# Optimization experiments

Hardware: AMD Instinct MI355X
Metric: run time of the kernel (lower is better)

The kernel has to match this reference:

```python
import jax, jax.numpy as jnp
import numpy as np

EPS = 1e-5

def layer_norm(x, g, b):
    m = jnp.mean(x, axis=-1, keepdims=True)
    v = jnp.mean((x - m) ** 2, axis=-1, keepdims=True)
    return (x - m) * jax.lax.rsqrt(v + EPS) * g + b

def conv1d(x, w, b, pad):
    # x: [B, C_in, L], w: [C_out, C_in, K]
    y = jax.lax.conv_general_dilated(x, w, (1,), [(pad, pad)],
                                     dimension_numbers=('NCH', 'OIH', 'NCH'))
    return y + b[None, :, None]

def setup_inputs() -> dict:
    key = jax.random.key(0)
    B, L, D, H, W, HID = 8, 1024, 512, 8, 3, 64
    ks = jax.random.split(key, 32)
    s = 0.02
    inp = {}
    inp['x'] = jax.random.normal(ks[0], (B, L, D), jnp.float32)
    # WaveDetector convs
    inp['conv1_w'] = jax.random.normal(ks[1], (HID, D, 5), jnp.float32) * s
    inp['conv1_b'] = jnp.zeros((HID,), jnp.float32)
    inp['conv2_w'] = jax.random.normal(ks[2], (HID, HID, 3), jnp.float32) * s
    inp['conv2_b'] = jnp.zeros((HID,), jnp.float32)
    inp['conv3_w'] = jax.random.normal(ks[3], (W, HID, 3), jnp.float32) * s
    inp['conv3_b'] = jnp.zeros((W,), jnp.float32)
    # wave type embedding
    inp['wave_emb'] = jax.random.normal(ks[4], (W, D), jnp.float32) * s
    # attention projections (stored as [in, out])
    inp['wq_w'] = jax.random.normal(ks[5], (D, D), jnp.float32) * s
    inp['wq_b'] = jnp.zeros((D,), jnp.float32)
    inp['wk_w'] = jax.random.normal(ks[6], (D, D), jnp.float32) * s
    inp['wk_b'] = jnp.zeros((D,), jnp.float32)
    inp['wv_w'] = jax.random.normal(ks[7], (D, D), jnp.float32) * s
    inp['wv_b'] = jnp.zeros((D,), jnp.float32)
    # gate MLP: D -> D//4 -> H
    inp['g1_w'] = jax.random.normal(ks[8], (D, D // 4), jnp.float32) * s
    inp['g1_b'] = jnp.zeros((D // 4,), jnp.float32)
    inp['g2_w'] = jax.random.normal(ks[9], (D // 4, H), jnp.float32) * s
    inp['g2_b'] = jnp.zeros((H,), jnp.float32)
    # layer norms
    for i, nm in enumerate(['ln_attn', 'norm1', 'ln_conv', 'norm2', 'norm3']):
        inp[nm + '_g'] = jnp.ones((D,), jnp.float32) + jax.random.normal(ks[10 + i], (D,), jnp.float32) * 0.01
        inp[nm + '_b'] = jax.random.normal(ks[15 + i], (D,), jnp.float32) * 0.01
    # subgraph conv: one Linear per wave + wave weights
    inp['wc_w'] = jax.random.normal(ks[20], (W, D, D), jnp.float32) * s
    inp['wc_b'] = jnp.zeros((W, D), jnp.float32)
    inp['wave_weights'] = jnp.ones((W,), jnp.float32) / W
    # FFN
    inp['f1_w'] = jax.random.normal(ks[21], (D, 4 * D), jnp.float32) * s
    inp['f1_b'] = jnp.zeros((4 * D,), jnp.float32)
    inp['f2_w'] = jax.random.normal(ks[22], (4 * D, D), jnp.float32) * s
    inp['f2_b'] = jnp.zeros((D,), jnp.float32)
    return inp

def reference(x, conv1_w, conv1_b, conv2_w, conv2_b, conv3_w, conv3_b, wave_emb,
              wq_w, wq_b, wk_w, wk_b, wv_w, wv_b, g1_w, g1_b, g2_w, g2_b,
              ln_attn_g, ln_attn_b, norm1_g, norm1_b, wc_w, wc_b, wave_weights,
              ln_conv_g, ln_conv_b, norm2_g, norm2_b, f1_w, f1_b, f2_w, f2_b,
              norm3_g, norm3_b):
    B, L, D = x.shape
    H = g2_w.shape[1]
    hd = D // H
    # --- WaveDetector ---
    xt = jnp.swapaxes(x, 1, 2)                       # [B, D, L]
    h = jax.nn.relu(conv1d(xt, conv1_w, conv1_b, 2))
    h = jax.nn.relu(conv1d(h, conv2_w, conv2_b, 1))
    wp = conv1d(h, conv3_w, conv3_b, 1)              # [B, W, L]
    wave_mask = jax.nn.softmax(jnp.swapaxes(wp, 1, 2), axis=-1)  # [B, L, W]
    # --- WaveTypeEncoding ---
    labels = jnp.argmax(wave_mask, axis=-1)          # [B, L] int
    x = x + wave_emb[labels]
    # --- subgraph adjacency (base_adj = ones) ---
    wave_sim = jnp.einsum('blw,bmw->blm', wave_mask, wave_mask)  # [B, L, L]
    subgraph_adj = wave_sim
    # --- DynamicWaveAttention ---
    residual = x
    Q = (x @ wq_w + wq_b).reshape(B, L, H, hd)
    K = (x @ wk_w + wk_b).reshape(B, L, H, hd)
    V = (x @ wv_w + wv_b).reshape(B, L, H, hd)
    scores = jnp.einsum('bqhd,bkhd->bhqk', Q, K) / (hd ** 0.5)
    gates = jax.nn.sigmoid(jax.nn.relu(x @ g1_w + g1_b) @ g2_w + g2_b)  # [B, L, H]
    gates = jnp.transpose(gates, (0, 2, 1))[:, :, None, :]              # [B, H, 1, L]
    scores = scores * gates + scores * wave_sim[:, None]
    scores = scores + subgraph_adj[:, None]
    attn = jax.nn.softmax(scores, axis=-1)
    attn_out = jnp.einsum('bhqk,bkhd->bqhd', attn, V).reshape(B, L, D)
    attn_out = layer_norm(attn_out + residual, ln_attn_g, ln_attn_b)
    x = layer_norm(x + attn_out, norm1_g, norm1_b)
    # --- ECGSubGraphConv (adj_matrices=None path) ---
    feats = jnp.einsum('bld,wdo->blwo', x, wc_w) + wc_b          # [B, L, W, D]
    conv_out = jnp.einsum('blwo,blw,w->blo', feats, wave_mask, wave_weights)
    conv_out = layer_norm(jax.nn.relu(conv_out), ln_conv_g, ln_conv_b)
    x = layer_norm(x + conv_out, norm2_g, norm2_b)
    # --- FFN ---
    ffn = jax.nn.relu(x @ f1_w + f1_b) @ f2_w + f2_b
    x = layer_norm(x + ffn, norm3_g, norm3_b)
    return (x, wave_mask, subgraph_adj)
```

## Files before the change

### kernel.cpp

```cpp
#include <hip/hip_runtime.h>

typedef unsigned short u16;
typedef unsigned int u32;
typedef __attribute__((ext_vector_type(8))) short bf16x8;
typedef __attribute__((ext_vector_type(4))) float f32x4;
typedef __attribute__((ext_vector_type(4))) u32 u32x4;

#define DEVI static __device__ __forceinline__

constexpr size_t OFF_WTQKV = 0;
constexpr size_t OFF_G1T   = 1572864;
constexpr size_t OFF_G2T   = OFF_G1T + 131072;
constexpr size_t OFF_WCT   = OFF_G2T + 2048;
constexpr size_t OFF_F1T   = OFF_WCT + 1572864;
constexpr size_t OFF_F2T   = OFF_F1T + 2097152;
constexpr size_t OFF_W1R   = OFF_F2T + 2097152;
constexpr size_t OFF_W2R   = OFF_W1R + 655360;
constexpr size_t OFF_H1    = OFF_W2R + 49152;
constexpr size_t OFF_GMID  = OFF_H1;
constexpr size_t OFF_GATES = OFF_H1 + 2097152;
constexpr size_t OFF_X1    = OFF_GATES + 262144;
constexpr size_t OFF_X3    = OFF_X1;
constexpr size_t OFF_X1B   = OFF_X1 + 16777216;
constexpr size_t OFF_FMID  = OFF_X1B;
constexpr size_t OFF_Q     = OFF_X1B + 8388608;
constexpr size_t OFF_H1P   = OFF_Q;
constexpr size_t OFF_K     = OFF_Q + 8388608;
constexpr size_t OFF_XH    = OFF_K;
constexpr size_t OFF_VT    = OFF_K + 8388608;
constexpr size_t OFF_XL    = OFF_VT + 32768;
constexpr size_t OFF_AO    = OFF_VT + 8388608;
constexpr size_t OFF_CONV  = OFF_AO;
constexpr size_t OFF_FP0   = OFF_AO;
constexpr size_t OFF_X2    = OFF_AO + 16777216;
constexpr size_t OFF_FP1   = OFF_X2;
constexpr size_t OFF_X2B   = OFF_X2 + 16777216;
constexpr size_t OFF_X3B   = OFF_X2B;

DEVI u16 f2bf(float f) {
  u32 u = __builtin_bit_cast(u32, f);
  u32 r = (u + 0x7FFFu + ((u >> 16) & 1u)) >> 16;
  return (u16)r;
}
DEVI float bf2f(u16 h) { u32 u = ((u32)h) << 16; return __builtin_bit_cast(float, u); }

DEVI void load8(const float* __restrict__ p, float o[8]) {
  const float4* q = (const float4*)p;
  float4 a = q[0], b = q[1];
  o[0]=a.x; o[1]=a.y; o[2]=a.z; o[3]=a.w; o[4]=b.x; o[5]=b.y; o[6]=b.z; o[7]=b.w;
}
DEVI void store8(float* __restrict__ p, const float o[8]) {
  float4 a; a.x=o[0]; a.y=o[1]; a.z=o[2]; a.w=o[3];
  float4 b; b.x=o[4]; b.y=o[5]; b.z=o[6]; b.w=o[7];
  float4* q = (float4*)p; q[0]=a; q[1]=b;
}
DEVI void store8bf(u16* __restrict__ p, const float o[8]) {
  u32 w[4];
#pragma unroll
  for (int i=0;i<4;i++) w[i] = (u32)f2bf(o[2*i]) | ((u32)f2bf(o[2*i+1]) << 16);
  u32x4 v; v.x=w[0]; v.y=w[1]; v.z=w[2]; v.w=w[3];
  *(u32x4*)p = v;
}

DEVI void gl_lds16(const u16* g, u16* l) {
  __builtin_amdgcn_global_load_lds((const __attribute__((address_space(1))) u32*)g,
                                   (__attribute__((address_space(3))) u32*)l, 16, 0, 0);
}

#define PIPE_WAIT(N)  asm volatile("s_waitcnt vmcnt(%0)" :: "n"(N) : "memory")
#define PIPE_WAIT0()  asm volatile("s_waitcnt vmcnt(0)" ::: "memory")
#define PIPE_BAR()    do { __builtin_amdgcn_s_barrier(); asm volatile("" ::: "memory"); } while (0)
#define PIPE_BAR_LGKM() do { asm volatile("s_waitcnt lgkmcnt(0)" ::: "memory"); \
                             __builtin_amdgcn_s_barrier(); asm volatile("" ::: "memory"); } while (0)

__global__ __launch_bounds__(64) void prep_kernel(
    const float* s0, const float* s1, const float* s2, const float* s3, const float* s4,
    const float* s5, const float* s6, const float* s7, const float* s8, const float* s9,
    char* ws) {
  const int jsrc[11] = {0,1,2,3,4, 5,5,5, 6,7, 9};
  const int jK[11]   = {512,512,512,512,128, 512,512,512, 512,2048, 64};
  const int jN[11]   = {512,512,512,128,8,   512,512,512, 2048,512, 192};
  const int jSo[11]  = {0,0,0,0,0, 0,262144,524288, 0,0, 0};
  const long long jDo[11] = {
    (long long)OFF_WTQKV, (long long)(OFF_WTQKV+524288), (long long)(OFF_WTQKV+1048576),
    (long long)OFF_G1T, (long long)OFF_G2T,
    (long long)OFF_WCT, (long long)(OFF_WCT+524288), (long long)(OFF_WCT+1048576),
    (long long)OFF_F1T, (long long)OFF_F2T, (long long)OFF_W2R};
  const int jF[11]   = {0,0,0,0,0,0,0,0,0,0,1};

  int blk = blockIdx.x;
  int j = 0, t = 0;
  for (int i = 0; i < 11; i++) {
    int cnt = ((jK[i] + 63) >> 6) * ((jN[i] + 63) >> 6);
    if (blk < cnt) { j = i; t = blk; break; }
    blk -= cnt;
  }
  int K = jK[j], N = jN[j];
  int ktiles = (K + 63) >> 6;
  int k0 = (t % ktiles) << 6, n0 = (t / ktiles) << 6;
  const float* SS[10] = {s0,s1,s2,s3,s4,s5,s6,s7,s8,s9};
  const float* src = SS[jsrc[j]] + jSo[j];
  __shared__ float tile[64][65];
  int tt = threadIdx.x;
  for (int i = 0; i < 64; i++) {
    float v = 0.f;
    if (k0 + i < K && n0 + tt < N) v = src[(size_t)(k0 + i) * N + n0 + tt];
    tile[i][tt] = v;
  }
  __syncthreads();
  if (jF[j]) {
    float* dst = (float*)(ws + jDo[j]);
    for (int i = 0; i < 64; i++)
      if (n0 + i < N && k0 + tt < K) dst[(size_t)(n0 + i) * K + k0 + tt] = tile[tt][i];
  } else {
    u16* dst = (u16*)(ws + jDo[j]);
    for (int i = 0; i < 64; i++)
      if (n0 + i < N && k0 + tt < K) dst[(size_t)(n0 + i) * K + k0 + tt] = f2bf(tile[tt][i]);
  }
}

__global__ __launch_bounds__(256) void wprep_kernel(const float* __restrict__ w1,
                                                    u16* __restrict__ wh, u16* __restrict__ wl) {
  int c = blockIdx.x;
  for (int kk = threadIdx.x; kk < 2560; kk += 256) {
    int k = kk >> 9, d = kk & 511;
    float v = w1[(size_t)c * 2560 + d * 5 + k];
    u16 h = f2bf(v);
    wh[(size_t)c * 2560 + kk] = h;
    wl[(size_t)c * 2560 + kk] = f2bf(v - bf2f(h));
  }
}

__global__ __launch_bounds__(256) void xsplit_kernel(const float* __restrict__ x,
                                                     u16* __restrict__ xh, u16* __restrict__ xl) {
  int idx = blockIdx.x * 256 + threadIdx.x;
  if (idx >= 8 * 1028 * 64) return;
  int r = idx >> 6;
  int col = (idx & 63) * 8;
  int b = r / 1028, rr = r % 1028;
  size_t dof = ((size_t)r) * 512 + col;
  if (rr < 2 || rr >= 1026) {
    u32x4 z; z.x = 0; z.y = 0; z.z = 0; z.w = 0;
    *(u32x4*)&xh[dof] = z;
    *(u32x4*)&xl[dof] = z;
    return;
  }
  const float* src = x + (((size_t)b << 10) + rr - 2) * 512 + col;
  float v[8];
  load8(src, v);
  u32 wh_[4], wl_[4];
#pragma unroll
  for (int i = 0; i < 4; i++) {
    u16 h0 = f2bf(v[2 * i]),     l0 = f2bf(v[2 * i]     - bf2f(f2bf(v[2 * i])));
    u16 h1 = f2bf(v[2 * i + 1]), l1 = f2bf(v[2 * i + 1] - bf2f(f2bf(v[2 * i + 1])));
    wh_[i] = (u32)h0 | ((u32)h1 << 16);
    wl_[i] = (u32)l0 | ((u32)l1 << 16);
  }
  u32x4 H; H.x=wh_[0]; H.y=wh_[1]; H.z=wh_[2]; H.w=wh_[3];
  u32x4 L; L.x=wl_[0]; L.y=wl_[1]; L.z=wl_[2]; L.w=wl_[3];
  *(u32x4*)&xh[dof] = H;
  *(u32x4*)&xl[dof] = L;
}

__global__ __launch_bounds__(256, 6) void conv1g_kernel(
    const u16* __restrict__ xh, const u16* __restrict__ xl,
    const u16* __restrict__ wh, const u16* __restrict__ wl,
    float* __restrict__ h1p) {
  __shared__ alignas(16) u16 a_s[2][64 * 32];
  __shared__ alignas(16) u16 b_s[2][64 * 32];
  const int tid = threadIdx.x, lane = tid & 63, wid = tid >> 6;
  const int m0 = blockIdx.x * 64;
  const int z = blockIdx.z;
  const int wr = wid >> 1, wc = wid & 1;
  const int mb = wr * 32, nb = wc * 32;
  const int lrow = lane & 15, lk = (lane >> 4) * 8;
  const int lr4 = lane >> 2, lc8 = (lane & 3) * 8;
  const int bb = m0 >> 10, lblk = m0 & 1023;
  const size_t xrow0 = (size_t)bb * 1028;

  auto stage = [&](int buf, int kk) {
    int p = (kk >= 5120) ? 2 : (kk >= 2560) ? 1 : 0;
    int kpp = kk - p * 2560;
    int ktap = kpp >> 9, d0 = kpp & 511;
    const u16* xa = (p == 1) ? xl : xh;
    const u16* wb = (p == 2) ? wl : wh;
    gl_lds16(&xa[(xrow0 + lblk + wid * 16 + lr4 + ktap) * 512 + d0 + lc8],
             &a_s[buf][wid * 512]);
    gl_lds16(&wb[(size_t)(wid * 16 + lr4) * 2560 + kpp + lc8],
             &b_s[buf][wid * 512]);
  };

  f32x4 acc[2][2];
#pragma unroll
  for (int m = 0; m < 2; m++)
#pragma unroll
    for (int n = 0; n < 2; n++) { acc[m][n].x=0.f; acc[m][n].y=0.f; acc[m][n].z=0.f; acc[m][n].w=0.f; }

  const int kz0 = z * 1920, kz1 = kz0 + 1920;
  stage(0, kz0);
  int cur = 0;
  for (int kk = kz0; kk < kz1; kk += 32) {
    if (kk + 32 < kz1) {
      stage(cur ^ 1, kk + 32);
      PIPE_WAIT(2);
    } else {
      PIPE_WAIT0();
    }
    PIPE_BAR();
    bf16x8 af[2], bfr[2];
#pragma unroll
    for (int m = 0; m < 2; m++) af[m]  = *(const bf16x8*)&a_s[cur][(mb + m * 16 + lrow) * 32 + lk];
#pragma unroll
    for (int n = 0; n < 2; n++) bfr[n] = *(const bf16x8*)&b_s[cur][(nb + n * 16 + lrow) * 32 + lk];
#pragma unroll
    for (int m = 0; m < 2; m++)
#pragma unroll
      for (int n = 0; n < 2; n++)
        acc[m][n] = __builtin_amdgcn_mfma_f32_16x16x32_bf16(af[m], bfr[n], acc[m][n], 0, 0, 0);
    PIPE_BAR_LGKM();
    cur ^= 1;
  }
  const int r4 = (lane >> 4) * 4;
#pragma unroll
  for (int m = 0; m < 2; m++) {
#pragma unroll
    for (int n = 0; n < 2; n++) {
      const int col = nb + n * 16 + lrow;
#pragma unroll
      for (int j = 0; j < 4; j++) {
        const int row = m0 + mb + m * 16 + r4 + j;
        h1p[(size_t)z * 524288 + (size_t)row * 64 + col] = acc[m][n][j];
      }
    }
  }
}

__global__ __launch_bounds__(256) void conv23_kernel(
    const float* __restrict__ h1p, const float* __restrict__ b1,
    const float* __restrict__ w2r, const float* __restrict__ b2,
    const float* __restrict__ w3, const float* __restrict__ b3,
    const float* __restrict__ x, const float* __restrict__ emb,
    float* __restrict__ wmOut, float* __restrict__ x1, u16* __restrict__ x1b) {
  int seg = blockIdx.x;
  int batch = seg >> 6, l0 = (seg & 63) << 4;
  int tid = threadIdx.x, lane = tid & 63, wave = tid >> 6;
  __shared__ float hs[20][64];
  __shared__ float h2s[18][65];
  __shared__ float w3s[576];
  __shared__ int labS[16];
  for (int i = tid; i < 20 * 64; i += 256) {
    int r = i >> 6, cc = i & 63;
    int lp = l0 - 2 + r;
    float v = 0.f;
    if (lp >= 0 && lp < 1024) {
      size_t base = ((size_t)batch * 1024 + lp) * 64 + cc;
      float s = b1[cc];
#pragma unroll
      for (int q = 0; q < 4; q++) s += h1p[base + (size_t)q * 524288];
      v = fmaxf(s, 0.f);
    }
    hs[r][cc] = v;
  }
  for (int i = tid; i < 576; i += 256) w3s[i] = w3[i];
  __syncthreads();
  {
    int c = lane;
    int r0 = wave * 5;
    float a2[5];
#pragma unroll
    for (int i = 0; i < 5; i++) a2[i] = b2[c];
    for (int dd = 0; dd < 64; dd++) {
      float xv[7];
#pragma unroll
      for (int i = 0; i < 7; i++) xv[i] = (r0 + i < 20) ? hs[r0 + i][dd] : 0.f;
#pragma unroll
      for (int k = 0; k < 3; k++) {
        float wv = w2r[(size_t)(dd * 3 + k) * 64 + c];
#pragma unroll
        for (int i = 0; i < 5; i++) a2[i] += xv[i + k] * wv;
      }
    }
#pragma unroll
    for (int i = 0; i < 5; i++) {
      int hr = r0 + i;
      if (hr < 18) h2s[hr][c] = fmaxf(a2[i], 0.f);
    }
  }
  __syncthreads();
  {
    int li = tid >> 4, g = tid & 15;
    int c0 = g * 4;
    float wp[3];
#pragma unroll
    for (int jw = 0; jw < 3; jw++) {
      float a = 0.f;
#pragma unroll
      for (int k = 0; k < 3; k++)
#pragma unroll
        for (int c = 0; c < 4; c++)
          a += h2s[li + k][c0 + c] * w3s[(jw * 64 + c0 + c) * 3 + k];
      wp[jw] = a;
    }
#pragma unroll
    for (int d = 1; d < 16; d <<= 1) {
#pragma unroll
      for (int jw = 0; jw < 3; jw++) wp[jw] += __shfl_xor(wp[jw], d);
    }
    if (g == 0) {
      float wp0 = wp[0] + b3[0], wp1 = wp[1] + b3[1], wp2 = wp[2] + b3[2];
      float mx = fmaxf(wp0, fmaxf(wp1, wp2));
      float e0 = __expf(wp0 - mx), e1 = __expf(wp1 - mx), e2 = __expf(wp2 - mx);
      float inv = 1.f / (e0 + e1 + e2);
      size_t mo = ((size_t)batch * 1024 + l0 + li) * 3;
      wmOut[mo] = e0 * inv; wmOut[mo + 1] = e1 * inv; wmOut[mo + 2] = e2 * inv;
      int lb = 0; float bv = wp0;
      if (wp1 > bv) { bv = wp1; lb = 1; }
      if (wp2 > bv) { lb = 2; }
      labS[li] = lb;
    }
  }
  __syncthreads();
  for (int i = tid; i < 16 * 128; i += 256) {
    int r = i >> 7, cq = (i & 127) << 2;
    size_t gi = ((size_t)batch * 1024 + l0 + r) * 512 + cq;
    float4 xv = *(const float4*)&x[gi];
    const float* ep = &emb[(size_t)labS[r] * 512 + cq];
    float4 ev = *(const float4*)ep;
    float4 v; v.x = xv.x + ev.x; v.y = xv.y + ev.y; v.z = xv.z + ev.z; v.w = xv.w + ev.w;
    *(float4*)&x1[gi] = v;
    u32 lo = (u32)f2bf(v.x) | ((u32)f2bf(v.y) << 16);
    u32 hi = (u32)f2bf(v.z) | ((u32)f2bf(v.w) << 16);
    *(u32*)&x1b[gi] = lo;
    *(u32*)&x1b[gi + 2] = hi;
  }
}

__global__ __launch_bounds__(256) void wavesim_kernel(const float* __restrict__ wm,
                                                      float* __restrict__ adj) {
  int b = blockIdx.x >> 7;
  int r0 = (blockIdx.x & 127) << 3;
  __shared__ float ms[1024][3];
  int tid = threadIdx.x;
  for (int i = tid; i < 3072; i += 256) ms[i / 3][i % 3] = wm[(size_t)b * 3072 + i];
  __syncthreads();
  for (int r = 0; r < 8; r++) {
    float a0 = ms[r0 + r][0], a1 = ms[r0 + r][1], a2 = ms[r0 + r][2];
    for (int m = tid; m < 1024; m += 256)
      adj[((size_t)b * 1024 + r0 + r) * 1024 + m] = a0 * ms[m][0] + a1 * ms[m][1] + a2 * ms[m][2];
  }
}

struct GemmArgs {
  const u16* A; const u16* Bt;
  int lda; int ldb; int K;
  const float* bias;
  u16* obf; int ldo;
  float* of32; int ldo32;
  u16* Qo; u16* Ko; u16* Vto;
  const float* bq; const float* bk; const float* bv;
};

template<int BM, int BN, int FM, int FN, int EPI>
__global__ __launch_bounds__(256, 3) void gemm_k(GemmArgs p) {
  __shared__ alignas(16) u16 a_s[2][BM * 32];
  __shared__ alignas(16) u16 b_s[2][BN * 32];
  const int tid = threadIdx.x;
  const int lane = tid & 63, wid = tid >> 6;
  const int m0 = blockIdx.x * BM, n0 = blockIdx.y * BN;
  const int koff = (EPI == 6) ? blockIdx.z * p.K : 0;
  const int wr = wid >> 1, wc = wid & 1;
  const int mb = wr * (FM * 16), nb = wc * (FN * 16);
  const int lrow = lane & 15, lk = (lane >> 4) * 8;
  constexpr int CPW_A = BM / 64;
  constexpr int CPW_B = BN / 64;
  constexpr int NL = CPW_A + CPW_B;
  const int lr4 = lane >> 2, lc8 = (lane & 3) * 8;

  auto stage = [&](int buf, int k0) {
#pragma unroll
    for (int j = 0; j < CPW_A; j++) {
      int chunk = wid * CPW_A + j;
      gl_lds16(&p.A[(size_t)(m0 + chunk * 16 + lr4) * p.lda + koff + k0 + lc8],
               &a_s[buf][chunk * 512]);
    }
#pragma unroll
    for (int j = 0; j < CPW_B; j++) {
      int chunk = wid * CPW_B + j;
      gl_lds16(&p.Bt[(size_t)(n0 + chunk * 16 + lr4) * p.ldb + koff + k0 + lc8],
               &b_s[buf][chunk * 512]);
    }
  };

  f32x4 acc[FM][FN];
#pragma unroll
  for (int m = 0; m < FM; m++)
#pragma unroll
    for (int n = 0; n < FN; n++) { acc[m][n].x=0.f; acc[m][n].y=0.f; acc[m][n].z=0.f; acc[m][n].w=0.f; }

  stage(0, 0);
  int cur = 0;
  for (int k0 = 0; k0 < p.K; k0 += 32) {
    if (k0 + 32 < p.K) {
      stage(cur ^ 1, k0 + 32);
      PIPE_WAIT(NL);
    } else {
      PIPE_WAIT0();
    }
    PIPE_BAR();
    bf16x8 af[FM], bfr[FN];
#pragma unroll
    for (int m = 0; m < FM; m++) af[m] = *(const bf16x8*)&a_s[cur][(mb + m * 16 + lrow) * 32 + lk];
#pragma unroll
    for (int n = 0; n < FN; n++) bfr[n] = *(const bf16x8*)&b_s[cur][(nb + n * 16 + lrow) * 32 + lk];
#pragma unroll
    for (int m = 0; m < FM; m++)
#pragma unroll
      for (int n = 0; n < FN; n++)
        acc[m][n] = __builtin_amdgcn_mfma_f32_16x16x32_bf16(af[m], bfr[n], acc[m][n], 0, 0, 0);
    PIPE_BAR_LGKM();
    cur ^= 1;
  }
  const int r4 = (lane >> 4) * 4;
#pragma unroll
  for (int m = 0; m < FM; m++) {
#pragma unroll
    for (int n = 0; n < FN; n++) {
      const int col = n0 + nb + n * 16 + lrow;
#pragma unroll
      for (int j = 0; j < 4; j++) {
        const int row = m0 + mb + m * 16 + r4 + j;
        float v = acc[m][n][j];
        if constexpr (EPI == 1) {
          v += p.bias[col];
          v = fmaxf(v, 0.f);
          p.obf[(size_t)row * p.ldo + col] = f2bf(v);
        } else if constexpr (EPI == 2) {
          v += p.bias[col];
          p.of32[(size_t)row * p.ldo32 + col] = v;
        } else if constexpr (EPI == 3) {
          if (col < 512) {
            v += p.bq[col];
            p.Qo[(size_t)row * 512 + col] = f2bf(v);
          } else if (col < 1024) {
            int cc = col - 512;
            v += p.bk[cc];
            p.Ko[(size_t)row * 512 + cc] = f2bf(v);
          } else if (col < 1536) {
            int cc = col - 1024;
            v += p.bv[cc];
            int hh = cc >> 6, dd = cc & 63;
            int bb2 = row >> 10, ll = row & 1023;
            p.Vto[((((size_t)bb2 * 8 + hh) * 64 + dd) << 10) + ll] = f2bf(v);
          } else {
            int cc = col - 1536;
            v += p.bias[cc];
            v = fmaxf(v, 0.f);
            p.obf[(size_t)row * 128 + cc] = f2bf(v);
          }
        } else if constexpr (EPI == 6) {
          if (blockIdx.z == 0) v += p.bias[col];
          p.of32[(size_t)blockIdx.z * p.ldo32 + (size_t)row * 512 + col] = v;
        }
      }
    }
  }
}

__global__ __launch_bounds__(256) void wcg_kernel(
    const u16* __restrict__ A, const u16* __restrict__ Wct,
    const float* __restrict__ wcb, const float* __restrict__ wmask,
    const float* __restrict__ wwts, float* __restrict__ out) {
  __shared__ alignas(16) u16 a_s[2][128 * 32];
  __shared__ alignas(16) u16 b_s[2][3 * 64 * 32];
  const int tid = threadIdx.x, lane = tid & 63, wid = tid >> 6;
  const int m0 = blockIdx.x * 128, n0 = blockIdx.y * 64;
  const int wr = wid >> 1, wc = wid & 1;
  const int mb = wr * 64, nb = wc * 32;
  const int lrow = lane & 15, lk = (lane >> 4) * 8;
  const int lr4 = lane >> 2, lc8 = (lane & 3) * 8;

  auto stage = [&](int buf, int k0) {
#pragma unroll
    for (int t = 0; t < 2; t++) {
      int ch = wid * 2 + t;
      gl_lds16(&A[(size_t)(m0 + ch * 16 + lr4) * 512 + k0 + lc8], &a_s[buf][ch * 512]);
    }
#pragma unroll
    for (int t = 0; t < 3; t++) {
      int ch = wid * 3 + t;
      int wI = ch >> 2, sub = ch & 3;
      gl_lds16(&Wct[(size_t)wI * 262144 + (size_t)(n0 + sub * 16 + lr4) * 512 + k0 + lc8],
               &b_s[buf][ch * 512]);
    }
  };

  f32x4 acc[4][2][3];
#pragma unroll
  for (int m = 0; m < 4; m++)
#pragma unroll
    for (int n = 0; n < 2; n++)
#pragma unroll
      for (int w = 0; w < 3; w++) { acc[m][n][w].x=0.f; acc[m][n][w].y=0.f; acc[m][n][w].z=0.f; acc[m][n][w].w=0.f; }

  stage(0, 0);
  int cur = 0;
  for (int k0 = 0; k0 < 512; k0 += 32) {
    if (k0 + 32 < 512) {
      stage(cur ^ 1, k0 + 32);
      PIPE_WAIT(5);
    } else {
      PIPE_WAIT0();
    }
    PIPE_BAR();
    bf16x8 af[4], bfr[3][2];
#pragma unroll
    for (int m = 0; m < 4; m++) af[m] = *(const bf16x8*)&a_s[cur][(mb + m * 16 + lrow) * 32 + lk];
#pragma unroll
    for (int w = 0; w < 3; w++)
#pragma unroll
      for (int n = 0; n < 2; n++)
        bfr[w][n] = *(const bf16x8*)&b_s[cur][(w * 64 + nb + n * 16 + lrow) * 32 + lk];
#pragma unroll
    for (int m = 0; m < 4; m++)
#pragma unroll
      for (int n = 0; n < 2; n++)
#pragma unroll
        for (int w = 0; w < 3; w++)
          acc[m][n][w] = __builtin_amdgcn_mfma_f32_16x16x32_bf16(af[m], bfr[w][n], acc[m][n][w], 0, 0, 0);
    PIPE_BAR_LGKM();
    cur ^= 1;
  }
  const float w0 = wwts[0], w1 = wwts[1], w2 = wwts[2];
  const int r4 = (lane >> 4) * 4;
#pragma unroll
  for (int m = 0; m < 4; m++) {
#pragma unroll
    for (int j = 0; j < 4; j++) {
      const int row = m0 + mb + m * 16 + r4 + j;
      float c0 = wmask[(size_t)row * 3 + 0] * w0;
      float c1 = wmask[(size_t)row * 3 + 1] * w1;
      float c2 = wmask[(size_t)row * 3 + 2] * w2;
#pragma unroll
      for (int n = 0; n < 2; n++) {
        const int col = n0 + nb + n * 16 + lrow;
        float v = c0 * (acc[m][n][0][j] + wcb[col])
                + c1 * (acc[m][n][1][j] + wcb[512 + col])
                + c2 * (acc[m][n][2][j] + wcb[1024 + col]);
        out[(size_t)row * 512 + col] = v;
      }
    }
  }
}

__global__ __launch_bounds__(256) void gates2_kernel(const u16* __restrict__ gmid,
    const u16* __restrict__ g2t, const float* __restrict__ g2b, float* __restrict__ gates) {
  int r0 = blockIdx.x * 64;
  __shared__ u16 ms[64][136];
  __shared__ u16 gs[8][136];
  __shared__ float gb[8];
  int tid = threadIdx.x;
  for (int i = tid; i < 1024; i += 256) {
    int r = i >> 4, ch = (i & 15) * 8;
    *(bf16x8*)&ms[r][ch] = *(const bf16x8*)&gmid[(size_t)(r0 + r) * 128 + ch];
  }
  if (tid < 128) {
    int r = tid >> 4, ch = (tid & 15) * 8;
    *(bf16x8*)&gs[r][ch] = *(const bf16x8*)&g2t[(size_t)r * 128 + ch];
  }
  if (tid < 8) gb[tid] = g2b[tid];
  __syncthreads();
  for (int o = tid; o < 512; o += 256) {
    int r = o >> 3, hh = o & 7;
    float a = gb[hh];
    for (int k = 0; k < 128; k++) a += bf2f(ms[r][k]) * bf2f(gs[hh][k]);
    gates[(size_t)(r0 + r) * 8 + hh] = 1.f / (1.f + __expf(-a));
  }
}

__global__ __launch_bounds__(256, 4) void attn_kernel(
    const u16* __restrict__ Qb, const u16* __restrict__ Kb, const u16* __restrict__ Vt,
    const float* __restrict__ gates, const float* __restrict__ wm, float* __restrict__ ao) {
  const int g = blockIdx.x & 63, qt = blockIdx.x >> 6;
  const int b = g >> 3, h = g & 7, q0 = qt << 6;
  const int tid = threadIdx.x, lane = tid & 63, w = tid >> 6;
  __shared__ alignas(16) u16 k_s[64 * 64];
  __shared__ alignas(16) u16 v_s[64 * 64];
  __shared__ u16 p_s[4][16][72];
  __shared__ float gat[64];
  __shared__ float wmk[64][4];
  const int lrow = lane & 15, lq = lane >> 4, lk = lq * 8;
  const int qrb = q0 + w * 16;
  const int sr_ = lane >> 3, sc_ = lane & 7;
  bf16x8 qf[2];
#pragma unroll
  for (int ks = 0; ks < 2; ks++)
    qf[ks] = *(const bf16x8*)&Qb[((size_t)(b * 1024 + qrb + lrow)) * 512 + h * 64 + ks * 32 + lk];
  float wq_[4][3];
#pragma unroll
  for (int j = 0; j < 4; j++) {
    int qr = qrb + lq * 4 + j;
#pragma unroll
    for (int t = 0; t < 3; t++) wq_[j][t] = wm[((size_t)b * 1024 + qr) * 3 + t];
  }
  float lsum[4];
  f32x4 oacc[4];
#pragma unroll
  for (int j = 0; j < 4; j++) lsum[j] = 0.f;
#pragma unroll
  for (int n = 0; n < 4; n++) { oacc[n].x=0.f; oacc[n].y=0.f; oacc[n].z=0.f; oacc[n].w=0.f; }

  const u16* Kbase = Kb + ((size_t)b * 1024) * 512 + h * 64;
  const u16* Vbase = Vt + ((size_t)(b * 8 + h)) * 64 * 1024;

  for (int kt = 0; kt < 16; kt++) {
    int k0 = kt * 64;
    __syncthreads();
#pragma unroll
    for (int t = 0; t < 2; t++) {
      int ch = (w << 1) | t;
      int r = (ch << 3) | sr_;
      int srcc = ((sc_ ^ (r & 7)) << 3);
      gl_lds16(&Kbase[(size_t)(k0 + r) * 512 + srcc], &k_s[ch << 9]);
      gl_lds16(&Vbase[(size_t)r * 1024 + k0 + srcc], &v_s[ch << 9]);
    }
    if (tid < 64) {
      gat[tid] = gates[((size_t)b * 1024 + k0 + tid) * 8 + h];
#pragma unroll
      for (int t = 0; t < 3; t++) wmk[tid][t] = wm[((size_t)b * 1024 + k0 + tid) * 3 + t];
    }
    __syncthreads();
    f32x4 s[4];
#pragma unroll
    for (int n = 0; n < 4; n++) { s[n].x=0.f; s[n].y=0.f; s[n].z=0.f; s[n].w=0.f; }
#pragma unroll
    for (int ks = 0; ks < 2; ks++) {
      bf16x8 kf[4];
#pragma unroll
      for (int n = 0; n < 4; n++) {
        int kr = n * 16 + lrow;
        kf[n] = *(const bf16x8*)&k_s[kr * 64 + ((((ks << 2) | lq) ^ (kr & 7)) << 3)];
      }
#pragma unroll
      for (int n = 0; n < 4; n++)
        s[n] = __builtin_amdgcn_mfma_f32_16x16x32_bf16(qf[ks], kf[n], s[n], 0, 0, 0);
    }
    float pv[4][4];
#pragma unroll
    for (int n = 0; n < 4; n++) {
      int cl = n * 16 + lrow;
      float gg = gat[cl];
      float w0 = wmk[cl][0], w1 = wmk[cl][1], w2 = wmk[cl][2];
#pragma unroll
      for (int j = 0; j < 4; j++) {
        float wsv = wq_[j][0] * w0 + wq_[j][1] * w1 + wq_[j][2] * w2;
        float sv = s[n][j] * 0.125f;
        float e = __expf(sv * (gg + wsv) + wsv);
        pv[n][j] = e;
        lsum[j] += e;
      }
    }
#pragma unroll
    for (int n = 0; n < 4; n++)
#pragma unroll
      for (int j = 0; j < 4; j++)
        p_s[w][lq * 4 + j][n * 16 + lrow] = f2bf(pv[n][j]);
#pragma unroll
    for (int ks = 0; ks < 2; ks++) {
      bf16x8 pa, vb[4];
      pa = *(const bf16x8*)&p_s[w][lrow][ks * 32 + lk];
#pragma unroll
      for (int n = 0; n < 4; n++) {
        int vr = n * 16 + lrow;
        vb[n] = *(const bf16x8*)&v_s[vr * 64 + ((((ks << 2) | lq) ^ (vr & 7)) << 3)];
      }
#pragma unroll
      for (int n = 0; n < 4; n++)
        oacc[n] = __builtin_amdgcn_mfma_f32_16x16x32_bf16(pa, vb[n], oacc[n], 0, 0, 0);
    }
  }
  float rinv[4];
#pragma unroll
  for (int j = 0; j < 4; j++) {
    float s = lsum[j];
#pragma unroll
    for (int d = 1; d < 16; d <<= 1) s += __shfl_xor(s, d);
    rinv[j] = 1.f / s;
  }
#pragma unroll
  for (int n = 0; n < 4; n++) {
    int col = h * 64 + n * 16 + lrow;
#pragma unroll
    for (int j = 0; j < 4; j++) {
      int row = b * 1024 + qrb + lq * 4 + j;
      ao[(size_t)row * 512 + col] = oacc[n][j] * rinv[j];
    }
  }
}

DEVI void ln512(const float u[8], const float* __restrict__ g, const float* __restrict__ b,
                int lane, float out[8]) {
  float s = 0.f;
#pragma unroll
  for (int i = 0; i < 8; i++) s += u[i];
#pragma unroll
  for (int m = 1; m < 64; m <<= 1) s += __shfl_xor(s, m);
  float mean = s * (1.f / 512.f);
  float d[8], q = 0.f;
#pragma unroll
  for (int i = 0; i < 8; i++) { d[i] = u[i] - mean; q += d[i] * d[i]; }
#pragma unroll
  for (int m = 1; m < 64; m <<= 1) q += __shfl_xor(q, m);
  float inv = rsqrtf(q * (1.f / 512.f) + 1e-5f);
  int base = lane * 8;
#pragma unroll
  for (int i = 0; i < 8; i++) out[i] = d[i] * inv * g[base + i] + b[base + i];
}

__global__ __launch_bounds__(256) void ln1_kernel(
    const float* __restrict__ ao, const float* __restrict__ x1,
    const float* __restrict__ ga, const float* __restrict__ gb,
    const float* __restrict__ n1g, const float* __restrict__ n1b,
    float* __restrict__ x2, u16* __restrict__ x2b) {
  int row = blockIdx.x * 4 + (threadIdx.x >> 6);
  int lane = threadIdx.x & 63;
  size_t base = (size_t)row * 512 + lane * 8;
  float av[8], xv[8], u[8], t[8];
  load8(ao + base, av);
  load8(x1 + base, xv);
#pragma unroll
  for (int i = 0; i < 8; i++) u[i] = av[i] + xv[i];
  ln512(u, ga, gb, lane, t);
#pragma unroll
  for (int i = 0; i < 8; i++) u[i] = xv[i] + t[i];
  ln512(u, n1g, n1b, lane, t);
  store8(x2 + base, t);
  store8bf(x2b + base, t);
}

__global__ __launch_bounds__(256) void ln2_kernel(
    const float* __restrict__ co, const float* __restrict__ x2,
    const float* __restrict__ gc, const float* __restrict__ bc,
    const float* __restrict__ n2g, const float* __restrict__ n2b,
    float* __restrict__ x3, u16* __restrict__ x3b) {
  int row = blockIdx.x * 4 + (threadIdx.x >> 6);
  int lane = threadIdx.x & 63;
  size_t base = (size_t)row * 512 + lane * 8;
  float av[8], xv[8], u[8], t[8];
  load8(co + base, av);
#pragma unroll
  for (int i = 0; i < 8; i++) u[i] = fmaxf(av[i], 0.f);
  ln512(u, gc, bc, lane, t);
  load8(x2 + base, xv);
#pragma unroll
  for (int i = 0; i < 8; i++) u[i] = xv[i] + t[i];
  ln512(u, n2g, n2b, lane, t);
  store8(x3 + base, t);
  store8bf(x3b + base, t);
}

__global__ __launch_bounds__(256) void ln3_kernel(
    const float* __restrict__ x3, const float* __restrict__ p0, const float* __restrict__ p1,
    const float* __restrict__ n3g, const float* __restrict__ n3b,
    float* __restrict__ out0) {
  int row = blockIdx.x * 4 + (threadIdx.x >> 6);
  int lane = threadIdx.x & 63;
  size_t base = (size_t)row * 512 + lane * 8;
  float a0[8], a1[8], xv[8], u[8], t[8];
  load8(x3 + base, xv);
  load8(p0 + base, a0);
  load8(p1 + base, a1);
#pragma unroll
  for (int i = 0; i < 8; i++) u[i] = xv[i] + a0[i] + a1[i];
  ln512(u, n3g, n3b, lane, t);
  store8(out0 + base, t);
}

extern "C" void kernel_launch(void* const* d_in, const int* in_sizes, int n_in,
                              void* d_out, int out_size, void* d_ws, size_t ws_size,
                              hipStream_t stream) {
  const float* x    = (const float*)d_in[0];
  const float* w1   = (const float*)d_in[1];
  const float* c1b  = (const float*)d_in[2];
  const float* w2   = (const float*)d_in[3];
  const float* c2b  = (const float*)d_in[4];
  const float* w3   = (const float*)d_in[5];
  const float* c3b  = (const float*)d_in[6];
  const float* emb  = (const float*)d_in[7];
  const float* wqw  = (const float*)d_in[8];
  const float* wqb  = (const float*)d_in[9];
  const float* wkw  = (const float*)d_in[10];
  const float* wkb  = (const float*)d_in[11];
  const float* wvw  = (const float*)d_in[12];
  const float* wvb  = (const float*)d_in[13];
  const float* g1w  = (const float*)d_in[14];
  const float* g1b  = (const float*)d_in[15];
  const float* g2w  = (const float*)d_in[16];
  const float* g2b  = (const float*)d_in[17];
  const float* lag  = (const float*)d_in[18];
  const float* lab  = (const float*)d_in[19];
  const float* n1g  = (const float*)d_in[20];
  const float* n1b  = (const float*)d_in[21];
  const float* lcg  = (const float*)d_in[22];
  const float* lcb  = (const float*)d_in[23];
  const float* n2g  = (const float*)d_in[24];
  const float* n2b  = (const float*)d_in[25];
  const float* n3g  = (const float*)d_in[26];
  const float* n3b  = (const float*)d_in[27];
  const float* wcw  = (const float*)d_in[28];
  const float* wcb  = (const float*)d_in[29];
  const float* wwts = (const float*)d_in[30];
  const float* f1w  = (const float*)d_in[31];
  const float* f1b  = (const float*)d_in[32];
  const float* f2w  = (const float*)d_in[33];
  const float* f2b  = (const float*)d_in[34];

  char* ws = (char*)d_ws;
  float* out0 = (float*)d_out;
  float* out1 = out0 + 4194304;
  float* out2 = out1 + 24576;

  float* w2r_p  = (float*)(ws + OFF_W2R);
  u16*   wh_p   = (u16*)(ws + OFF_W1R);
  u16*   wl_p   = (u16*)(ws + OFF_W1R + 327680);
  u16*   xh_p   = (u16*)(ws + OFF_XH);
  u16*   xl_p   = (u16*)(ws + OFF_XL);
  float* h1p_p  = (float*)(ws + OFF_H1P);
  float* x1_p   = (float*)(ws + OFF_X1);
  u16*   x1b_p  = (u16*)(ws + OFF_X1B);
  u16*   wtqkv  = (u16*)(ws + OFF_WTQKV);
  u16*   g2t_p  = (u16*)(ws + OFF_G2T);
  u16*   wct_p  = (u16*)(ws + OFF_WCT);
  u16*   f1t_p  = (u16*)(ws + OFF_F1T);
  u16*   f2t_p  = (u16*)(ws + OFF_F2T);
  u16*   q_p    = (u16*)(ws + OFF_Q);
  u16*   k_p    = (u16*)(ws + OFF_K);
  u16*   vt_p   = (u16*)(ws + OFF_VT);
  u16*   gmid_p = (u16*)(ws + OFF_GMID);
  float* gates_p= (float*)(ws + OFF_GATES);
  float* ao_p   = (float*)(ws + OFF_AO);
  float* x2_p   = (float*)(ws + OFF_X2);
  u16*   x2b_p  = (u16*)(ws + OFF_X2B);
  float* conv_p = (float*)(ws + OFF_CONV);
  float* x3_p   = (float*)(ws + OFF_X3);
  u16*   x3b_p  = (u16*)(ws + OFF_X3B);
  u16*   fmid_p = (u16*)(ws + OFF_FMID);
  float* fp0_p  = (float*)(ws + OFF_FP0);
  float* fp1_p  = (float*)(ws + OFF_FP1);

  prep_kernel<<<917, 64, 0, stream>>>(wqw, wkw, wvw, g1w, g2w, wcw, f1w, f2w, w1, w2, ws);
  wprep_kernel<<<64, 256, 0, stream>>>(w1, wh_p, wl_p);
  xsplit_kernel<<<2056, 256, 0, stream>>>(x, xh_p, xl_p);
  conv1g_kernel<<<dim3(128, 1, 4), 256, 0, stream>>>(xh_p, xl_p, wh_p, wl_p, h1p_p);
  conv23_kernel<<<512, 256, 0, stream>>>(h1p_p, c1b, w2r_p, c2b, w3, c3b, x, emb, out1, x1_p, x1b_p);
  wavesim_kernel<<<1024, 256, 0, stream>>>(out1, out2);
  {
    GemmArgs a{}; a.A = x1b_p; a.lda = 512; a.Bt = wtqkv; a.ldb = 512; a.K = 512;
    a.Qo = q_p; a.Ko = k_p; a.Vto = vt_p; a.bq = wqb; a.bk = wkb; a.bv = wvb;
    a.bias = g1b; a.obf = gmid_p; a.ldo = 128;
    gemm_k<128,128,4,4,3><<<dim3(64,13), 256, 0, stream>>>(a);
  }
  gates2_kernel<<<128, 256, 0, stream>>>(gmid_p, g2t_p, g2b, gates_p);
  attn_kernel<<<1024, 256, 0, stream>>>(q_p, k_p, vt_p, gates_p, out1, ao_p);
  ln1_kernel<<<2048, 256, 0, stream>>>(ao_p, x1_p, lag, lab, n1g, n1b, x2_p, x2b_p);
  wcg_kernel<<<dim3(64, 8), 256, 0, stream>>>(x2b_p, wct_p, wcb, out1, wwts, conv_p);
  ln2_kernel<<<2048, 256, 0, stream>>>(conv_p, x2_p, lcg, lcb, n2g, n2b, x3_p, x3b_p);
  {
    GemmArgs a{}; a.A = x3b_p; a.lda = 512; a.Bt = f1t_p; a.ldb = 512; a.K = 512;
    a.bias = f1b; a.obf = fmid_p; a.ldo = 2048;
    gemm_k<128,128,4,4,1><<<dim3(64,16), 256, 0, stream>>>(a);
  }
  {
    GemmArgs a{}; a.A = fmid_p; a.lda = 2048; a.Bt = f2t_p; a.ldb = 2048; a.K = 1024;
    a.bias = f2b; a.of32 = fp0_p; a.ldo32 = 4194304;
    gemm_k<128,128,4,4,6><<<dim3(64,4,2), 256, 0, stream>>>(a);
  }
  ln3_kernel<<<2048, 256, 0, stream>>>(x3_p, fp0_p, fp1_p, n3g, n3b, out0);

  (void)in_sizes; (void)n_in; (void)out_size; (void)ws_size;
}
```

Baseline: 308.5 us.

## Double-buffer K/V and gate tiles in attention with async global-to-LDS loads

The attention kernel now double-buffers the K, V, gate and wave-mask tiles in shared memory. The next tile is prefetched with global_load_lds while the current one is being computed, and vmcnt waits replace the two __syncthreads per iteration. The gate and wave-mask loads also move from per-thread register loads to direct LDS loads, with the wave-mask stored transposed. Shared memory roughly doubles, so launch bounds drop to 3 blocks per CU, which may reduce occupancy.

```diff
diff --git a/kernel.cpp b/kernel.cpp
--- a/kernel.cpp
+++ b/kernel.cpp
@@ -65,6 +65,10 @@
 DEVI void gl_lds16(const u16* g, u16* l) {
   __builtin_amdgcn_global_load_lds((const __attribute__((address_space(1))) u32*)g,
                                    (__attribute__((address_space(3))) u32*)l, 16, 0, 0);
+}
+DEVI void gl_lds4(const float* g, float* l) {
+  __builtin_amdgcn_global_load_lds((const __attribute__((address_space(1))) u32*)g,
+                                   (__attribute__((address_space(3))) u32*)l, 4, 0, 0);
 }
 
 #define PIPE_WAIT(N)  asm volatile("s_waitcnt vmcnt(%0)" :: "n"(N) : "memory")
@@ -577,17 +581,17 @@
   }
 }
 
-__global__ __launch_bounds__(256, 4) void attn_kernel(
+__global__ __launch_bounds__(256, 3) void attn_kernel(
     const u16* __restrict__ Qb, const u16* __restrict__ Kb, const u16* __restrict__ Vt,
     const float* __restrict__ gates, const float* __restrict__ wm, float* __restrict__ ao) {
   const int g = blockIdx.x & 63, qt = blockIdx.x >> 6;
   const int b = g >> 3, h = g & 7, q0 = qt << 6;
   const int tid = threadIdx.x, lane = tid & 63, w = tid >> 6;
-  __shared__ alignas(16) u16 k_s[64 * 64];
-  __shared__ alignas(16) u16 v_s[64 * 64];
+  __shared__ alignas(16) u16 k_s[2][64 * 64];
+  __shared__ alignas(16) u16 v_s[2][64 * 64];
   __shared__ u16 p_s[4][16][72];
-  __shared__ float gat[64];
-  __shared__ float wmk[64][4];
+  __shared__ float gat[2][64];
+  __shared__ float wmk[2][3][64];
   const int lrow = lane & 15, lq = lane >> 4, lk = lq * 8;
   const int qrb = q0 + w * 16;
   const int sr_ = lane >> 3, sc_ = lane & 7;
@@ -611,24 +615,36 @@
 
   const u16* Kbase = Kb + ((size_t)b * 1024) * 512 + h * 64;
   const u16* Vbase = Vt + ((size_t)(b * 8 + h)) * 64 * 1024;
-
-  for (int kt = 0; kt < 16; kt++) {
+  const float* Gbase = gates + ((size_t)b * 1024) * 8 + h;
+  const float* Wbase = wm + ((size_t)b * 1024) * 3;
+
+  auto stage = [&](int buf, int kt) {
     int k0 = kt * 64;
-    __syncthreads();
 #pragma unroll
     for (int t = 0; t < 2; t++) {
       int ch = (w << 1) | t;
       int r = (ch << 3) | sr_;
       int srcc = ((sc_ ^ (r & 7)) << 3);
-      gl_lds16(&Kbase[(size_t)(k0 + r) * 512 + srcc], &k_s[ch << 9]);
-      gl_lds16(&Vbase[(size_t)r * 1024 + k0 + srcc], &v_s[ch << 9]);
-    }
-    if (tid < 64) {
-      gat[tid] = gates[((size_t)b * 1024 + k0 + tid) * 8 + h];
-#pragma unroll
-      for (int t = 0; t < 3; t++) wmk[tid][t] = wm[((size_t)b * 1024 + k0 + tid) * 3 + t];
-    }
-    __syncthreads();
+      gl_lds16(&Kbase[(size_t)(k0 + r) * 512 + srcc], &k_s[buf][ch << 9]);
+      gl_lds16(&Vbase[(size_t)r * 1024 + k0 + srcc], &v_s[buf][ch << 9]);
+    }
+    if (w == 0) {
+      gl_lds4(&Gbase[(size_t)(k0 + lane) * 8], &gat[buf][0]);
+    } else {
+      gl_lds4(&Wbase[(size_t)(k0 + lane) * 3 + (w - 1)], &wmk[buf][w - 1][0]);
+    }
+  };
+
+  stage(0, 0);
+  int buf = 0;
+  for (int kt = 0; kt < 16; kt++) {
+    if (kt + 1 < 16) {
+      stage(buf ^ 1, kt + 1);
+      PIPE_WAIT(5);
+    } else {
+      PIPE_WAIT0();
+    }
+    PIPE_BAR();
     f32x4 s[4];
 #pragma unroll
     for (int n = 0; n < 4; n++) { s[n].x=0.f; s[n].y=0.f; s[n].z=0.f; s[n].w=0.f; }
@@ -638,7 +654,7 @@
 #pragma unroll
       for (int n = 0; n < 4; n++) {
         int kr = n * 16 + lrow;
-        kf[n] = *(const bf16x8*)&k_s[kr * 64 + ((((ks << 2) | lq) ^ (kr & 7)) << 3)];
+        kf[n] = *(const bf16x8*)&k_s[buf][kr * 64 + ((((ks << 2) | lq) ^ (kr & 7)) << 3)];
       }
 #pragma unroll
       for (int n = 0; n < 4; n++)
@@ -648,8 +664,8 @@
 #pragma unroll
     for (int n = 0; n < 4; n++) {
       int cl = n * 16 + lrow;
-      float gg = gat[cl];
-      float w0 = wmk[cl][0], w1 = wmk[cl][1], w2 = wmk[cl][2];
+      float gg = gat[buf][cl];
+      float w0 = wmk[buf][0][cl], w1 = wmk[buf][1][cl], w2 = wmk[buf][2][cl];
 #pragma unroll
       for (int j = 0; j < 4; j++) {
         float wsv = wq_[j][0] * w0 + wq_[j][1] * w1 + wq_[j][2] * w2;
@@ -671,12 +687,14 @@
 #pragma unroll
       for (int n = 0; n < 4; n++) {
         int vr = n * 16 + lrow;
-        vb[n] = *(const bf16x8*)&v_s[vr * 64 + ((((ks << 2) | lq) ^ (vr & 7)) << 3)];
+        vb[n] = *(const bf16x8*)&v_s[buf][vr * 64 + ((((ks << 2) | lq) ^ (vr & 7)) << 3)];
       }
 #pragma unroll
       for (int n = 0; n < 4; n++)
         oacc[n] = __builtin_amdgcn_mfma_f32_16x16x32_bf16(pa, vb[n], oacc[n], 0, 0, 0);
     }
+    PIPE_BAR_LGKM();
+    buf ^= 1;
   }
   float rinv[4];
 #pragma unroll
```

New measurement: 317.7 us. 1.03x slower.
